# Optimization experiments

Measured on AMD Instinct MI355X. Metric: run time of the kernel, lower is better.

The kernel has to match this reference:

```python
import jax, jax.numpy as jnp
import numpy as np

B, S, D = 2, 2048, 2048
H = 16
I = 8192  # intermediate_size
HD = I // H  # per-head intermediate dim = 512


def setup_inputs() -> dict:
    key = jax.random.key(0)
    ks = jax.random.split(key, 7)
    scale_d = 1.0 / np.sqrt(D)
    scale_i = 1.0 / np.sqrt(I)
    return {
        "x": jax.random.normal(ks[0], (B, S, D), dtype=jnp.float32),
        "adjacency": jax.random.uniform(ks[1], (B, H, S, S), dtype=jnp.float32) * (1.0 / S),
        "Wg": jax.random.normal(ks[2], (D, I), dtype=jnp.float32) * scale_d,
        "Wu": jax.random.normal(ks[3], (D, I), dtype=jnp.float32) * scale_d,
        "Wd": jax.random.normal(ks[4], (I, D), dtype=jnp.float32) * scale_i,
        "eps": jnp.zeros((H,), dtype=jnp.float32),
        "alpha": jnp.ones((H,), dtype=jnp.float32),
    }


def reference(x, adjacency, Wg, Wu, Wd, eps, alpha):
    # gate/up projections + SwiGLU: (B,S,I)
    gate = jnp.einsum("bsd,di->bsi", x, Wg)
    up = jnp.einsum("bsd,di->bsi", x, Wu)
    h_inter = jax.nn.silu(gate) * up
    # split into heads: (B,H,S,HD)
    h_heads = h_inter.reshape(B, S, H, HD).transpose(0, 2, 1, 3)
    # batched per-head GIN: (1+eps_h)*h + alpha_h * A_h @ h, all heads at once
    agg = jnp.einsum("bhst,bhtd->bhsd", adjacency, h_heads)
    e = (1.0 + eps)[None, :, None, None]
    a = alpha[None, :, None, None]
    h_gin = e * h_heads + a * agg
    # recombine heads -> (B,S,I), then down projection
    h_comb = h_gin.transpose(0, 2, 1, 3).reshape(B, S, I)
    return jnp.einsum("bsi,id->bsd", h_comb, Wd)
```

## Files before the change

### kernel.cpp

```cpp
#include <hip/hip_runtime.h>
#include <hip/hip_bf16.h>


typedef __bf16 bf16x8 __attribute__((ext_vector_type(8)));
typedef float f32x4 __attribute__((ext_vector_type(4)));

__device__ __forceinline__ unsigned short f2bf(float f) {
    union { float f; unsigned int u; } x; x.f = f;
    unsigned int r = x.u + 0x7fffu + ((x.u >> 16) & 1u);
    return (unsigned short)(r >> 16);
}
__device__ __forceinline__ float bf2f(unsigned short b) {
    union { unsigned int u; float f; } x; x.u = ((unsigned int)b) << 16;
    return x.f;
}

__device__ __forceinline__ void gload_lds16(const void* g, void* l) {
    __builtin_amdgcn_global_load_lds((const __attribute__((address_space(1))) void*)g,
                                     (__attribute__((address_space(3))) void*)l,
                                     16, 0, 0);
}


__global__ void conv_kernel(const float* __restrict__ in, unsigned short* __restrict__ out) {
    size_t i = ((size_t)blockIdx.x * 256 + threadIdx.x) * 4;
    float4 v = *(const float4*)(in + i);
    ushort4 o; o.x = f2bf(v.x); o.y = f2bf(v.y); o.z = f2bf(v.z); o.w = f2bf(v.w);
    *(ushort4*)(out + i) = o;
}

__global__ void tconv_kernel(const float* __restrict__ in, unsigned short* __restrict__ out,
                             int R, int C) {
    __shared__ float tile[64][65];
    int nbc = C >> 6;
    int bc = blockIdx.x % nbc, br = blockIdx.x / nbc;
    int r0 = br * 64, c0 = bc * 64;
    int t = threadIdx.x;
#pragma unroll
    for (int i = 0; i < 4; ++i) {
        int idx = i * 256 + t;
        int r = idx >> 4, c4 = (idx & 15) * 4;
        float4 v = *(const float4*)(in + (size_t)(r0 + r) * C + c0 + c4);
        tile[r][c4] = v.x; tile[r][c4 + 1] = v.y; tile[r][c4 + 2] = v.z; tile[r][c4 + 3] = v.w;
    }
    __syncthreads();
#pragma unroll
    for (int i = 0; i < 4; ++i) {
        int idx = i * 256 + t;
        int c = idx >> 4, r4 = (idx & 15) * 4;
        ushort4 o;
        o.x = f2bf(tile[r4][c]); o.y = f2bf(tile[r4 + 1][c]);
        o.z = f2bf(tile[r4 + 2][c]); o.w = f2bf(tile[r4 + 3][c]);
        *(ushort4*)(out + (size_t)(c0 + c) * R + r0 + r4) = o;
    }
}

template<int EPI>
__global__ void __launch_bounds__(512, 2) gemm256(
    const unsigned short* __restrict__ Ag,
    const unsigned short* __restrict__ Bg,
    const unsigned short* __restrict__ gbuf_c,
    unsigned short* __restrict__ gbuf,
    unsigned short* __restrict__ hhT)
{
    const int K = 2048;
    __shared__ unsigned short LDS[4][16384];
    int bid = (int)blockIdx.x;
    int lb = (bid & 7) * 64 + (bid >> 3);
    int nt = lb & 31, mt = lb >> 5;
    int tid = threadIdx.x, lane = tid & 63, wave = tid >> 6;
    int wm = wave >> 2, wn = wave & 3;
    int l15 = lane & 15, l4 = lane >> 4;

    f32x4 acc[8][4] = {};

    int jl = (lane & 7) ^ (lane >> 3);
    int prow0 = wave * 16 + (lane >> 3);
    int row0 = prow0 + ((jl & 4) << 5);
    int cc = (jl & 3) << 3;
    const unsigned short* srcA0 = Ag + (size_t)(mt * 256 + row0) * K + cc;
    const unsigned short* srcA1 = srcA0 + (size_t)8 * K;
    const unsigned short* srcB0 = Bg + (size_t)(nt * 256 + row0) * K + cc;
    const unsigned short* srcB1 = srcB0 + (size_t)8 * K;

    int cA = l15 * 128 + (((l4 + wm * 4) ^ (l15 & 7)) << 4);
    int cB = ((wn & 1) * 64 + l15) * 128 + (((l4 + ((wn >> 1) << 2)) ^ (l15 & 7)) << 4);

#define STAGE_A(t_) do { char* d_ = (char*)&LDS[(t_) & 3][0] + wave * 2048;              \
        gload_lds16((const void*)(srcA0 + (size_t)(t_) * 32), (void*)d_);                \
        gload_lds16((const void*)(srcA1 + (size_t)(t_) * 32), (void*)(d_ + 1024)); } while (0)
#define STAGE_B(t_) do { char* d_ = (char*)&LDS[(t_) & 3][8192] + wave * 2048;           \
        gload_lds16((const void*)(srcB0 + (size_t)(t_) * 32), (void*)d_);                \
        gload_lds16((const void*)(srcB1 + (size_t)(t_) * 32), (void*)(d_ + 1024)); } while (0)

    STAGE_A(0); STAGE_B(0);
    STAGE_A(1); STAGE_B(1);

    for (int t = 0; t < 64; ++t) {
        if (t + 2 < 64) asm volatile("s_waitcnt vmcnt(4)" ::: "memory");
        else            asm volatile("s_waitcnt vmcnt(0)" ::: "memory");
        __builtin_amdgcn_s_barrier();
        const char* Abase = (const char*)&LDS[t & 3][0];
        const char* Bbase = Abase + 16384;
        bool more = (t + 2) < 64;
        if (more) STAGE_A(t + 2);
        bf16x8 bf[4], af[4];
#pragma unroll
        for (int ni = 0; ni < 4; ++ni) bf[ni] = *(const bf16x8*)(Bbase + cB + ni * 2048);
#pragma unroll
        for (int mi = 0; mi < 4; ++mi) af[mi] = *(const bf16x8*)(Abase + cA + mi * 2048);
        __builtin_amdgcn_s_setprio(1);
#pragma unroll
        for (int mi = 0; mi < 4; ++mi)
#pragma unroll
            for (int ni = 0; ni < 4; ++ni)
                acc[mi][ni] = __builtin_amdgcn_mfma_f32_16x16x32_bf16(af[mi], bf[ni], acc[mi][ni], 0, 0, 0);
        __builtin_amdgcn_s_setprio(0);
        if (more) STAGE_B(t + 2);
#pragma unroll
        for (int mi = 0; mi < 4; ++mi) af[mi] = *(const bf16x8*)(Abase + cA + 8192 + mi * 2048);
        __builtin_amdgcn_s_setprio(1);
#pragma unroll
        for (int mi = 0; mi < 4; ++mi)
#pragma unroll
            for (int ni = 0; ni < 4; ++ni)
                acc[4 + mi][ni] = __builtin_amdgcn_mfma_f32_16x16x32_bf16(af[mi], bf[ni], acc[4 + mi][ni], 0, 0, 0);
        __builtin_amdgcn_s_setprio(0);
    }
#undef STAGE_A
#undef STAGE_B

    if (EPI == 0) {
        ushort4* g4 = (ushort4*)gbuf;
        size_t base = ((size_t)lb * 32) * 512 + tid;
#pragma unroll
        for (int a = 0; a < 8; ++a)
#pragma unroll
            for (int ni = 0; ni < 4; ++ni) {
                f32x4 v = acc[a][ni];
                ushort4 o;
                o.x = f2bf(v[0]); o.y = f2bf(v[1]); o.z = f2bf(v[2]); o.w = f2bf(v[3]);
                g4[base + (size_t)(a * 4 + ni) * 512] = o;
            }
    } else {
        const ushort4* g4 = (const ushort4*)gbuf_c;
        size_t base = ((size_t)lb * 32) * 512 + tid;
        int rowb = mt * 256 + wm * 128 + l4 * 4;
        int colb = nt * 256 + wn * 64 + l15;
        int b = mt >> 3;
#pragma unroll
        for (int a = 0; a < 8; ++a)
#pragma unroll
            for (int ni = 0; ni < 4; ++ni) {
                ushort4 gq = g4[base + (size_t)(a * 4 + ni) * 512];
                int row = rowb + a * 16;
                int n = colb + ni * 16;
                ushort4 hv;
#pragma unroll
                for (int r = 0; r < 4; ++r) {
                    float gv = bf2f(((const unsigned short*)&gq)[r]);
                    float u = acc[a][ni][r];
                    float h = gv / (1.f + __expf(-gv)) * u;
                    ((unsigned short*)&hv)[r] = f2bf(h);
                }
                *(ushort4*)(hhT + ((size_t)b * 8192 + n) * 2048 + (row & 2047)) = hv;
            }
    }
}

__global__ void __launch_bounds__(512, 2) gemm_agg3(
    const float* __restrict__ adj,
    const unsigned short* __restrict__ hhT,
    const float* __restrict__ eps, const float* __restrict__ alpha,
    unsigned short* __restrict__ hcomb)
{
    const int S = 2048, HD = 512, I = 8192;
    __shared__ unsigned short As[2][128 * 40];
    __shared__ unsigned short Bs[2][512 * 40];
    int bid = (int)blockIdx.x;
    int lb = (bid & 7) * 64 + (bid >> 3);
    int pair = lb >> 4;
    int mt = lb & 15;
    int b = pair >> 4, h = pair & 15;
    int tid = threadIdx.x;
    int lane = tid & 63;
    int wave = tid >> 6;
    int wm = wave >> 2, wn = wave & 3;
    f32x4 acc[4][8] = {};

    float e1 = 1.f + eps[h];
    float a1 = alpha[h];
    bool a1z = (a1 == 0.f);
    float dfac = a1z ? 0.f : (e1 / a1);

    const float* Ab = adj + ((size_t)pair * S + (size_t)mt * 128) * S;
    const unsigned short* Bb = hhT + ((size_t)b * I + (size_t)h * HD) * (size_t)S;

    int a_row0 = tid >> 3, a_c = (tid & 7) << 2;
    int grow0 = mt * 128 + a_row0;
    int b_row0 = tid >> 2, b_ch = (tid & 3) << 3;

    float4 pa0_0, pa1_0, pa0_1, pa1_1;
    int4 pb0_0, pb1_0, pb2_0, pb3_0, pb0_1, pb1_1, pb2_1, pb3_1;

#define AGG_LOAD(SET, K0)                                                               \
    do {                                                                                \
        pa0_##SET = *(const float4*)(Ab + (size_t)a_row0 * S + (K0) + a_c);             \
        pa1_##SET = *(const float4*)(Ab + (size_t)(a_row0 + 64) * S + (K0) + a_c);      \
        pb0_##SET = *(const int4*)(Bb + (size_t)b_row0 * S + (K0) + b_ch);              \
        pb1_##SET = *(const int4*)(Bb + (size_t)(b_row0 + 128) * S + (K0) + b_ch);      \
        pb2_##SET = *(const int4*)(Bb + (size_t)(b_row0 + 256) * S + (K0) + b_ch);      \
        pb3_##SET = *(const int4*)(Bb + (size_t)(b_row0 + 384) * S + (K0) + b_ch);      \
    } while (0)

#define AGG_WRITE(SET, BUF, K0)                                                         \
    do {                                                                                \
        int j0 = grow0 - (K0) - a_c;                                                    \
        pa0_##SET.x += (j0 == 0) ? dfac : 0.f;                                          \
        pa0_##SET.y += (j0 == 1) ? dfac : 0.f;                                          \
        pa0_##SET.z += (j0 == 2) ? dfac : 0.f;                                          \
        pa0_##SET.w += (j0 == 3) ? dfac : 0.f;                                          \
        int j1 = j0 + 64;                                                               \
        pa1_##SET.x += (j1 == 0) ? dfac : 0.f;                                          \
        pa1_##SET.y += (j1 == 1) ? dfac : 0.f;                                          \
        pa1_##SET.z += (j1 == 2) ? dfac : 0.f;                                          \
        pa1_##SET.w += (j1 == 3) ? dfac : 0.f;                                          \
        ushort4 o0, o1;                                                                 \
        o0.x = f2bf(pa0_##SET.x); o0.y = f2bf(pa0_##SET.y);                             \
        o0.z = f2bf(pa0_##SET.z); o0.w = f2bf(pa0_##SET.w);                             \
        o1.x = f2bf(pa1_##SET.x); o1.y = f2bf(pa1_##SET.y);                             \
        o1.z = f2bf(pa1_##SET.z); o1.w = f2bf(pa1_##SET.w);                             \
        *(ushort4*)((char*)As[BUF] + a_row0 * 80 + a_c * 2) = o0;                       \
        *(ushort4*)((char*)As[BUF] + (a_row0 + 64) * 80 + a_c * 2) = o1;                \
        *(int4*)((char*)Bs[BUF] + b_row0 * 80 + b_ch * 2) = pb0_##SET;                  \
        *(int4*)((char*)Bs[BUF] + (b_row0 + 128) * 80 + b_ch * 2) = pb1_##SET;          \
        *(int4*)((char*)Bs[BUF] + (b_row0 + 256) * 80 + b_ch * 2) = pb2_##SET;          \
        *(int4*)((char*)Bs[BUF] + (b_row0 + 384) * 80 + b_ch * 2) = pb3_##SET;          \
    } while (0)

    int lrow = lane & 15;
    int koff2 = ((lane >> 4) << 3) * 2;
    const char* aptr0 = (const char*)As[0] + (wm * 64 + lrow) * 80 + koff2;
    const char* bptr0 = (const char*)Bs[0] + (wn * 128 + lrow) * 80 + koff2;
    const char* aptr1 = (const char*)As[1] + (wm * 64 + lrow) * 80 + koff2;
    const char* bptr1 = (const char*)Bs[1] + (wn * 128 + lrow) * 80 + koff2;

#define AGG_COMPUTE(APTR, BPTR)                                                         \
    do {                                                                                \
        bf16x8 af[4], bfv[8];                                                           \
        _Pragma("unroll")                                                               \
        for (int mi = 0; mi < 4; ++mi) af[mi] = *(const bf16x8*)((APTR) + mi * 16 * 80);\
        _Pragma("unroll")                                                               \
        for (int ni = 0; ni < 8; ++ni) bfv[ni] = *(const bf16x8*)((BPTR) + ni * 16 * 80);\
        __builtin_amdgcn_s_setprio(1);                                                  \
        _Pragma("unroll")                                                               \
        for (int mi = 0; mi < 4; ++mi)                                                  \
            _Pragma("unroll")                                                           \
            for (int ni = 0; ni < 8; ++ni)                                              \
                acc[mi][ni] = __builtin_amdgcn_mfma_f32_16x16x32_bf16(af[mi], bfv[ni],  \
                                                                      acc[mi][ni], 0, 0, 0); \
        __builtin_amdgcn_s_setprio(0);                                                  \
    } while (0)

    AGG_LOAD(0, 0);
    AGG_WRITE(0, 0, 0);
    AGG_LOAD(1, 32);
    asm volatile("s_waitcnt lgkmcnt(0)" ::: "memory");
    __builtin_amdgcn_s_barrier();

    for (int s = 0; s < 64; s += 2) {
        if (s + 2 < 64) AGG_LOAD(0, (s + 2) * 32);
        AGG_COMPUTE(aptr0, bptr0);
        AGG_WRITE(1, 1, (s + 1) * 32);
        asm volatile("s_waitcnt lgkmcnt(0)" ::: "memory");
        __builtin_amdgcn_s_barrier();
        if (s + 3 < 64) AGG_LOAD(1, (s + 3) * 32);
        AGG_COMPUTE(aptr1, bptr1);
        if (s + 2 < 64) {
            AGG_WRITE(0, 0, (s + 2) * 32);
            asm volatile("s_waitcnt lgkmcnt(0)" ::: "memory");
            __builtin_amdgcn_s_barrier();
        }
    }
#undef AGG_LOAD
#undef AGG_WRITE
#undef AGG_COMPUTE

    int s_base = mt * 128 + wm * 64;
    int d_base = wn * 128;
    if (!a1z) {
#pragma unroll
        for (int mi = 0; mi < 4; ++mi)
#pragma unroll
            for (int ni = 0; ni < 8; ++ni) {
                int sb = s_base + mi * 16 + ((lane >> 4) << 2);
                int d = d_base + ni * 16 + (lane & 15);
#pragma unroll
                for (int r = 0; r < 4; ++r) {
                    size_t off = ((size_t)(b * S + sb + r)) * I + (size_t)h * HD + d;
                    hcomb[off] = f2bf(a1 * acc[mi][ni][r]);
                }
            }
    } else {
#pragma unroll
        for (int mi = 0; mi < 4; ++mi)
#pragma unroll
            for (int ni = 0; ni < 8; ++ni) {
                int sb = s_base + mi * 16 + ((lane >> 4) << 2);
                int d = d_base + ni * 16 + (lane & 15);
                size_t col = (size_t)h * HD + d;
                ushort4 hq = *(const ushort4*)(hhT + ((size_t)b * I + col) * S + sb);
#pragma unroll
                for (int r = 0; r < 4; ++r) {
                    size_t off = ((size_t)(b * S + sb + r)) * I + col;
                    hcomb[off] = f2bf(e1 * bf2f(((const unsigned short*)&hq)[r]));
                }
            }
    }
}

__global__ void __launch_bounds__(512, 2) gemm_out2(
    const unsigned short* __restrict__ hcomb,
    const unsigned short* __restrict__ WdT,
    float* __restrict__ out)
{
    const int K = 8192;
    __shared__ unsigned short LDS[6][12288];
    int bid = (int)blockIdx.x;
    int lb = (bid & 7) * 32 + (bid >> 3);
    int mt = lb >> 4, nt = lb & 15;
    int tid = threadIdx.x, lane = tid & 63, wave = tid >> 6;
    int wm = wave >> 1, wn = wave & 1;
    int l15 = lane & 15, l4 = lane >> 4;
    f32x4 acc[4][4] = {};

    int jl = (lane & 7) ^ (lane >> 3);
    int prowA = wave * 16 + (lane >> 3);
    int rowA0 = prowA + ((jl & 4) << 5);
    int ccA = (jl & 3) << 3;
    const unsigned short* srcA0 = hcomb + (size_t)(mt * 256 + rowA0) * K + ccA;
    const unsigned short* srcA1 = srcA0 + (size_t)8 * K;
    int prowB = tid >> 3;
    int jbl = (tid & 7) ^ (prowB & 7);
    int rowB0 = prowB + ((jbl & 4) << 4);
    int ccB = (jbl & 3) << 3;
    const unsigned short* srcB0 = WdT + (size_t)(nt * 128 + rowB0) * K + ccB;

    int cA0 = ((wm & 1) * 64 + l15) * 128 + (((((wm >> 1) << 2) + l4) ^ (l15 & 7)) << 4);
    int cB0 = l15 * 128 + ((((wn << 2) + l4) ^ (l15 & 7)) << 4);

#define OSTAGE(t_) do {                                                                  \
        char* dA = (char*)&LDS[(t_) % 6][0] + wave * 2048;                               \
        gload_lds16((const void*)(srcA0 + (size_t)(t_) * 32), (void*)dA);                \
        gload_lds16((const void*)(srcA1 + (size_t)(t_) * 32), (void*)(dA + 1024));       \
        char* dB = (char*)&LDS[(t_) % 6][8192] + wave * 1024;                            \
        gload_lds16((const void*)(srcB0 + (size_t)(t_) * 32), (void*)dB);                \
    } while (0)

    OSTAGE(0); OSTAGE(1); OSTAGE(2); OSTAGE(3);

    for (int t = 0; t < 256; ++t) {
        if (t + 3 < 256)      asm volatile("s_waitcnt vmcnt(9)" ::: "memory");
        else if (t + 2 < 256) asm volatile("s_waitcnt vmcnt(6)" ::: "memory");
        else if (t + 1 < 256) asm volatile("s_waitcnt vmcnt(3)" ::: "memory");
        else                  asm volatile("s_waitcnt vmcnt(0)" ::: "memory");
        __builtin_amdgcn_s_barrier();
        const char* Abase = (const char*)&LDS[t % 6][0];
        const char* Bbase = Abase + 16384;
        bool more = (t + 4) < 256;
        bf16x8 af[4], bf[4];
#pragma unroll
        for (int ni = 0; ni < 4; ++ni) bf[ni] = *(const bf16x8*)(Bbase + cB0 + ni * 2048);
        if (more) OSTAGE(t + 4);
#pragma unroll
        for (int mi = 0; mi < 4; ++mi) af[mi] = *(const bf16x8*)(Abase + cA0 + mi * 2048);
        __builtin_amdgcn_s_setprio(1);
#pragma unroll
        for (int mi = 0; mi < 4; ++mi)
#pragma unroll
            for (int ni = 0; ni < 4; ++ni)
                acc[mi][ni] = __builtin_amdgcn_mfma_f32_16x16x32_bf16(af[mi], bf[ni], acc[mi][ni], 0, 0, 0);
        __builtin_amdgcn_s_setprio(0);
    }
#undef OSTAGE

    int m_off = mt * 256 + wm * 64, n_off = nt * 128 + wn * 64;
#pragma unroll
    for (int mi = 0; mi < 4; ++mi)
#pragma unroll
        for (int ni = 0; ni < 4; ++ni) {
            int mbase = m_off + mi * 16 + l4 * 4;
            int n = n_off + ni * 16 + l15;
#pragma unroll
            for (int r = 0; r < 4; ++r)
                out[(size_t)(mbase + r) * 2048 + n] = acc[mi][ni][r];
        }
}

extern "C" void kernel_launch(void* const* d_in, const int* in_sizes, int n_in,
                              void* d_out, int out_size, void* d_ws, size_t ws_size,
                              hipStream_t stream) {
    const float* x     = (const float*)d_in[0];
    const float* adj   = (const float*)d_in[1];
    const float* Wg    = (const float*)d_in[2];
    const float* Wu    = (const float*)d_in[3];
    const float* Wd    = (const float*)d_in[4];
    const float* eps   = (const float*)d_in[5];
    const float* alpha = (const float*)d_in[6];
    float* out = (float*)d_out;

    unsigned short* ws    = (unsigned short*)d_ws;
    unsigned short* xb    = ws;
    unsigned short* WgT   = xb + (size_t)4096 * 2048;
    unsigned short* WuT   = WgT + (size_t)8192 * 2048;
    unsigned short* WdT   = WuT + (size_t)8192 * 2048;
    unsigned short* hhT   = WdT + (size_t)2048 * 8192;
    unsigned short* hcomb = hhT + (size_t)16384 * 2048;
    unsigned short* gbuf  = hcomb;

    conv_kernel<<<8192, 256, 0, stream>>>(x, xb);
    tconv_kernel<<<4096, 256, 0, stream>>>(Wg, WgT, 2048, 8192);
    tconv_kernel<<<4096, 256, 0, stream>>>(Wu, WuT, 2048, 8192);
    tconv_kernel<<<4096, 256, 0, stream>>>(Wd, WdT, 8192, 2048);
    gemm256<0><<<512, 512, 0, stream>>>(xb, WgT, nullptr, gbuf, nullptr);
    gemm256<1><<<512, 512, 0, stream>>>(xb, WuT, gbuf, nullptr, hhT);
    gemm_agg3<<<512, 512, 0, stream>>>(adj, hhT, eps, alpha, hcomb);
    gemm_out2<<<256, 512, 0, stream>>>(hcomb, WdT, out);
}
```

Measured before the change: 719.1 us.

## Stream aggregation B tiles via direct global-to-LDS loads and deepen GEMM prefetch

The aggregation GEMM now loads its hhT operand straight into LDS with global_load_lds into a 4-deep swizzled ring buffer. This replaces the register-staged loads and LDS stores, and the B fragment reads use a XOR swizzle. The A (adjacency) path keeps register staging with the fp32-to-bf16 conversion, and it is reordered to sit alongside the B staging. The projection GEMM prefetch distance also goes from 2 to 3 stages, with adjusted vmcnt waits. The aim is to cut VGPR pressure and LDS store traffic and to hide more memory latency. The risk is that the LDS-DMA completion is only ordered implicitly, through vmcnt waits on the A register loads.

```diff
diff --git a/kernel.cpp b/kernel.cpp
--- a/kernel.cpp
+++ b/kernel.cpp
@@ -95,15 +95,17 @@
 
     STAGE_A(0); STAGE_B(0);
     STAGE_A(1); STAGE_B(1);
+    STAGE_A(2); STAGE_B(2);
 
     for (int t = 0; t < 64; ++t) {
-        if (t + 2 < 64) asm volatile("s_waitcnt vmcnt(4)" ::: "memory");
-        else            asm volatile("s_waitcnt vmcnt(0)" ::: "memory");
+        if (t + 2 < 64)      asm volatile("s_waitcnt vmcnt(8)" ::: "memory");
+        else if (t + 1 < 64) asm volatile("s_waitcnt vmcnt(4)" ::: "memory");
+        else                 asm volatile("s_waitcnt vmcnt(0)" ::: "memory");
         __builtin_amdgcn_s_barrier();
         const char* Abase = (const char*)&LDS[t & 3][0];
         const char* Bbase = Abase + 16384;
-        bool more = (t + 2) < 64;
-        if (more) STAGE_A(t + 2);
+        bool more = (t + 3) < 64;
+        if (more) STAGE_A(t + 3);
         bf16x8 bf[4], af[4];
 #pragma unroll
         for (int ni = 0; ni < 4; ++ni) bf[ni] = *(const bf16x8*)(Bbase + cB + ni * 2048);
@@ -116,7 +118,7 @@
             for (int ni = 0; ni < 4; ++ni)
                 acc[mi][ni] = __builtin_amdgcn_mfma_f32_16x16x32_bf16(af[mi], bf[ni], acc[mi][ni], 0, 0, 0);
         __builtin_amdgcn_s_setprio(0);
-        if (more) STAGE_B(t + 2);
+        if (more) STAGE_B(t + 3);
 #pragma unroll
         for (int mi = 0; mi < 4; ++mi) af[mi] = *(const bf16x8*)(Abase + cA + 8192 + mi * 2048);
         __builtin_amdgcn_s_setprio(1);
@@ -168,7 +170,7 @@
     }
 }
 
-__global__ void __launch_bounds__(512, 2) gemm_agg3(
+__global__ void __launch_bounds__(512, 2) gemm_agg4(
     const float* __restrict__ adj,
     const unsigned short* __restrict__ hhT,
     const float* __restrict__ eps, const float* __restrict__ alpha,
@@ -176,16 +178,15 @@
 {
     const int S = 2048, HD = 512, I = 8192;
     __shared__ unsigned short As[2][128 * 40];
-    __shared__ unsigned short Bs[2][512 * 40];
+    __shared__ unsigned short Bs[4][512 * 32];
     int bid = (int)blockIdx.x;
     int lb = (bid & 7) * 64 + (bid >> 3);
     int pair = lb >> 4;
     int mt = lb & 15;
     int b = pair >> 4, h = pair & 15;
-    int tid = threadIdx.x;
-    int lane = tid & 63;
-    int wave = tid >> 6;
+    int tid = threadIdx.x, lane = tid & 63, wave = tid >> 6;
     int wm = wave >> 2, wn = wave & 3;
+    int l15 = lane & 15, l4 = lane >> 4;
     f32x4 acc[4][8] = {};
 
     float e1 = 1.f + eps[h];
@@ -198,60 +199,63 @@
 
     int a_row0 = tid >> 3, a_c = (tid & 7) << 2;
     int grow0 = mt * 128 + a_row0;
-    int b_row0 = tid >> 2, b_ch = (tid & 3) << 3;
+
+    int jl = (lane & 7) ^ (lane >> 3);
+    int prow0 = wave * 16 + (lane >> 3);
+    int browB = prow0 + ((jl & 4) << 6);
+    int ccB = (jl & 3) << 3;
+    const unsigned short* srcB = Bb + (size_t)browB * S + ccB;
+
+#define BSTAGE(t_) do {                                                           \
+        char* d_ = (char*)&Bs[(t_) & 3][0] + wave * 2048;                         \
+        const unsigned short* s_ = srcB + (size_t)(t_) * 32;                      \
+        gload_lds16((const void*)s_, (void*)d_);                                  \
+        gload_lds16((const void*)(s_ + (size_t)8 * S), (void*)(d_ + 1024));       \
+        gload_lds16((const void*)(s_ + (size_t)128 * S), (void*)(d_ + 16384));    \
+        gload_lds16((const void*)(s_ + (size_t)136 * S), (void*)(d_ + 17408));    \
+    } while (0)
 
     float4 pa0_0, pa1_0, pa0_1, pa1_1;
-    int4 pb0_0, pb1_0, pb2_0, pb3_0, pb0_1, pb1_1, pb2_1, pb3_1;
-
-#define AGG_LOAD(SET, K0)                                                               \
-    do {                                                                                \
-        pa0_##SET = *(const float4*)(Ab + (size_t)a_row0 * S + (K0) + a_c);             \
-        pa1_##SET = *(const float4*)(Ab + (size_t)(a_row0 + 64) * S + (K0) + a_c);      \
-        pb0_##SET = *(const int4*)(Bb + (size_t)b_row0 * S + (K0) + b_ch);              \
-        pb1_##SET = *(const int4*)(Bb + (size_t)(b_row0 + 128) * S + (K0) + b_ch);      \
-        pb2_##SET = *(const int4*)(Bb + (size_t)(b_row0 + 256) * S + (K0) + b_ch);      \
-        pb3_##SET = *(const int4*)(Bb + (size_t)(b_row0 + 384) * S + (K0) + b_ch);      \
+
+#define ALOAD(SET, K0)                                                            \
+    do {                                                                          \
+        pa0_##SET = *(const float4*)(Ab + (size_t)a_row0 * S + (K0) + a_c);       \
+        pa1_##SET = *(const float4*)(Ab + (size_t)(a_row0 + 64) * S + (K0) + a_c);\
     } while (0)
 
-#define AGG_WRITE(SET, BUF, K0)                                                         \
-    do {                                                                                \
-        int j0 = grow0 - (K0) - a_c;                                                    \
-        pa0_##SET.x += (j0 == 0) ? dfac : 0.f;                                          \
-        pa0_##SET.y += (j0 == 1) ? dfac : 0.f;                                          \
-        pa0_##SET.z += (j0 == 2) ? dfac : 0.f;                                          \
-        pa0_##SET.w += (j0 == 3) ? dfac : 0.f;                                          \
-        int j1 = j0 + 64;                                                               \
-        pa1_##SET.x += (j1 == 0) ? dfac : 0.f;                                          \
-        pa1_##SET.y += (j1 == 1) ? dfac : 0.f;                                          \
-        pa1_##SET.z += (j1 == 2) ? dfac : 0.f;                                          \
-        pa1_##SET.w += (j1 == 3) ? dfac : 0.f;                                          \
-        ushort4 o0, o1;                                                                 \
-        o0.x = f2bf(pa0_##SET.x); o0.y = f2bf(pa0_##SET.y);                             \
-        o0.z = f2bf(pa0_##SET.z); o0.w = f2bf(pa0_##SET.w);                             \
-        o1.x = f2bf(pa1_##SET.x); o1.y = f2bf(pa1_##SET.y);                             \
-        o1.z = f2bf(pa1_##SET.z); o1.w = f2bf(pa1_##SET.w);                             \
-        *(ushort4*)((char*)As[BUF] + a_row0 * 80 + a_c * 2) = o0;                       \
-        *(ushort4*)((char*)As[BUF] + (a_row0 + 64) * 80 + a_c * 2) = o1;                \
-        *(int4*)((char*)Bs[BUF] + b_row0 * 80 + b_ch * 2) = pb0_##SET;                  \
-        *(int4*)((char*)Bs[BUF] + (b_row0 + 128) * 80 + b_ch * 2) = pb1_##SET;          \
-        *(int4*)((char*)Bs[BUF] + (b_row0 + 256) * 80 + b_ch * 2) = pb2_##SET;          \
-        *(int4*)((char*)Bs[BUF] + (b_row0 + 384) * 80 + b_ch * 2) = pb3_##SET;          \
+#define ACONV(SET, BUF, K0)                                                       \
+    do {                                                                          \
+        int j0 = grow0 - (K0) - a_c;                                              \
+        pa0_##SET.x += (j0 == 0) ? dfac : 0.f;                                    \
+        pa0_##SET.y += (j0 == 1) ? dfac : 0.f;                                    \
+        pa0_##SET.z += (j0 == 2) ? dfac : 0.f;                                    \
+        pa0_##SET.w += (j0 == 3) ? dfac : 0.f;                                    \
+        int j1 = j0 + 64;                                                         \
+        pa1_##SET.x += (j1 == 0) ? dfac : 0.f;                                    \
+        pa1_##SET.y += (j1 == 1) ? dfac : 0.f;                                    \
+        pa1_##SET.z += (j1 == 2) ? dfac : 0.f;                                    \
+        pa1_##SET.w += (j1 == 3) ? dfac : 0.f;                                    \
+        ushort4 o0, o1;                                                           \
+        o0.x = f2bf(pa0_##SET.x); o0.y = f2bf(pa0_##SET.y);                       \
+        o0.z = f2bf(pa0_##SET.z); o0.w = f2bf(pa0_##SET.w);                       \
+        o1.x = f2bf(pa1_##SET.x); o1.y = f2bf(pa1_##SET.y);                       \
+        o1.z = f2bf(pa1_##SET.z); o1.w = f2bf(pa1_##SET.w);                       \
+        *(ushort4*)((char*)As[BUF] + a_row0 * 80 + a_c * 2) = o0;                 \
+        *(ushort4*)((char*)As[BUF] + (a_row0 + 64) * 80 + a_c * 2) = o1;          \
     } while (0)
 
-    int lrow = lane & 15;
-    int koff2 = ((lane >> 4) << 3) * 2;
-    const char* aptr0 = (const char*)As[0] + (wm * 64 + lrow) * 80 + koff2;
-    const char* bptr0 = (const char*)Bs[0] + (wn * 128 + lrow) * 80 + koff2;
-    const char* aptr1 = (const char*)As[1] + (wm * 64 + lrow) * 80 + koff2;
-    const char* bptr1 = (const char*)Bs[1] + (wn * 128 + lrow) * 80 + koff2;
-
-#define AGG_COMPUTE(APTR, BPTR)                                                         \
+    int koff2 = l4 << 4;
+    const char* aptr0 = (const char*)As[0] + (wm * 64 + l15) * 80 + koff2;
+    const char* aptr1 = (const char*)As[1] + (wm * 64 + l15) * 80 + koff2;
+    int cB = ((wn & 1) * 128 + l15) * 128 + (((l4 + ((wn >> 1) << 2)) ^ (l15 & 7)) << 4);
+
+#define AGG_COMPUTE(APTR, BBASE)                                                        \
     do {                                                                                \
         bf16x8 af[4], bfv[8];                                                           \
         _Pragma("unroll")                                                               \
         for (int mi = 0; mi < 4; ++mi) af[mi] = *(const bf16x8*)((APTR) + mi * 16 * 80);\
         _Pragma("unroll")                                                               \
-        for (int ni = 0; ni < 8; ++ni) bfv[ni] = *(const bf16x8*)((BPTR) + ni * 16 * 80);\
+        for (int ni = 0; ni < 8; ++ni) bfv[ni] = *(const bf16x8*)((BBASE) + cB + ni * 2048);\
         __builtin_amdgcn_s_setprio(1);                                                  \
         _Pragma("unroll")                                                               \
         for (int mi = 0; mi < 4; ++mi)                                                  \
@@ -262,28 +266,34 @@
         __builtin_amdgcn_s_setprio(0);                                                  \
     } while (0)
 
-    AGG_LOAD(0, 0);
-    AGG_WRITE(0, 0, 0);
-    AGG_LOAD(1, 32);
+    BSTAGE(0);
+    ALOAD(0, 0);
+    BSTAGE(1);
+    ALOAD(1, 32);
+    BSTAGE(2);
+    ACONV(0, 0, 0);
     asm volatile("s_waitcnt lgkmcnt(0)" ::: "memory");
     __builtin_amdgcn_s_barrier();
 
     for (int s = 0; s < 64; s += 2) {
-        if (s + 2 < 64) AGG_LOAD(0, (s + 2) * 32);
-        AGG_COMPUTE(aptr0, bptr0);
-        AGG_WRITE(1, 1, (s + 1) * 32);
+        AGG_COMPUTE(aptr0, (const char*)&Bs[s & 3][0]);
+        ACONV(1, 1, (s + 1) * 32);
+        if (s + 2 < 64) ALOAD(0, (s + 2) * 32);
+        if (s + 3 < 64) BSTAGE(s + 3);
         asm volatile("s_waitcnt lgkmcnt(0)" ::: "memory");
         __builtin_amdgcn_s_barrier();
-        if (s + 3 < 64) AGG_LOAD(1, (s + 3) * 32);
-        AGG_COMPUTE(aptr1, bptr1);
+        AGG_COMPUTE(aptr1, (const char*)&Bs[(s + 1) & 3][0]);
         if (s + 2 < 64) {
-            AGG_WRITE(0, 0, (s + 2) * 32);
+            ACONV(0, 0, (s + 2) * 32);
+            if (s + 3 < 64) ALOAD(1, (s + 3) * 32);
+            if (s + 4 < 64) BSTAGE(s + 4);
             asm volatile("s_waitcnt lgkmcnt(0)" ::: "memory");
             __builtin_amdgcn_s_barrier();
         }
     }
-#undef AGG_LOAD
-#undef AGG_WRITE
+#undef BSTAGE
+#undef ALOAD
+#undef ACONV
 #undef AGG_COMPUTE
 
     int s_base = mt * 128 + wm * 64;
@@ -424,6 +434,6 @@
     tconv_kernel<<<4096, 256, 0, stream>>>(Wd, WdT, 8192, 2048);
     gemm256<0><<<512, 512, 0, stream>>>(xb, WgT, nullptr, gbuf, nullptr);
     gemm256<1><<<512, 512, 0, stream>>>(xb, WuT, gbuf, nullptr, hhT);
-    gemm_agg3<<<512, 512, 0, stream>>>(adj, hhT, eps, alpha, hcomb);
+    gemm_agg4<<<512, 512, 0, stream>>>(adj, hhT, eps, alpha, hcomb);
     gemm_out2<<<256, 512, 0, stream>>>(hcomb, WdT, out);
 }
```

Result: no change. 719.5 us (+0.1%).
